# Kernel tuning notes

Measured on AMD Instinct MI355X. Metric: run time of the kernel, lower is better.

The kernel has to match this reference:

```python
import jax, jax.numpy as jnp
import numpy as np
import math

NUM_LEVEL = 16
LEVEL_DIM = 2
BASE_RES = 16
LOG2_T = 19
LEVEL_SCALE = 1.38191288
N_POINTS = 262144

_PRIMES = np.array([1, 2654435761, 805459861], dtype=np.uint32)  # tiny-cuda-nn hash primes
_CORNERS = np.array([[(c >> d) & 1 for d in range(3)] for c in range(8)], dtype=np.uint32)  # [8,3]


def _grid_meta():
    # mirrors GridEncoder.get_grid_info: per-level table offsets (aligned to 8)
    max_len = 2 ** LOG2_T
    offs = []
    off = 0
    for i in range(NUM_LEVEL):
        res = int(np.ceil(BASE_RES * LEVEL_SCALE ** i))
        p = min(max_len, res ** 3)
        p = int(np.ceil(p / 8) * 8)
        offs.append(off)
        off += p
    offs.append(off)
    return offs


def setup_inputs() -> dict:
    key = jax.random.key(0)
    k1, k2 = jax.random.split(key)
    offs = _grid_meta()
    # raw coords in [-1, 1); forward maps (x+1)/2 -> [0, 1)
    input_means = jax.random.uniform(k1, (N_POINTS, 3), dtype=jnp.float32) * 2.0 - 1.0
    # embeddings.data.uniform_(-0.01, 0.01)
    embeddings = jax.random.uniform(k2, (offs[-1], LEVEL_DIM), dtype=jnp.float32) * 0.02 - 0.01
    return {"input_means": input_means, "embeddings": embeddings}


def _encode(input_means, embeddings):
    x = (input_means + 1.0) / 2.0  # [N,3] in [0,1]
    offs = _grid_meta()
    lg_scale = math.log2(LEVEL_SCALE)
    corners = jnp.asarray(_CORNERS)  # [8,3]
    primes = jnp.asarray(_PRIMES)    # [3]
    outs = []
    for l in range(NUM_LEVEL):
        hsize = offs[l + 1] - offs[l]                    # table rows this level
        scale = 2.0 ** (l * lg_scale) * BASE_RES - 1.0   # align_corners=True
        res = int(math.ceil(scale)) + 1                  # grid resolution
        table = embeddings[offs[l]:offs[l + 1]]          # [hsize, C]
        pos = x * scale                                  # align_corners -> no +0.5
        pg = jnp.floor(pos)
        frac = pos - pg                                  # [N,3]
        pgu = pg.astype(jnp.uint32)
        cpos = pgu[:, None, :] + corners[None]           # [N,8,3] corner coords
        if res ** 3 > hsize:
            # hashed level: xor of coord*prime (uint32 wraparound)
            h = cpos * primes
            idx = h[..., 0] ^ h[..., 1] ^ h[..., 2]
        else:
            # dense (tiled) level
            r = jnp.uint32(res)
            idx = cpos[..., 0] + cpos[..., 1] * r + cpos[..., 2] * r * r
        idx = (idx % jnp.uint32(hsize)).astype(jnp.int32)
        feats = table[idx]                               # [N,8,C] gather
        w = jnp.where(corners[None] == 1, frac[:, None, :], 1.0 - frac[:, None, :]).prod(-1)  # [N,8]
        outs.append(jnp.einsum('nk,nkc->nc', w, feats))  # trilinear interp
    # matches ot_encod.permute(1,0,2).reshape(N, L*C): level-major feature concat
    return jnp.concatenate(outs, axis=-1)                # [N, L*C]


def reference(input_means, embeddings):
    return _encode(input_means, embeddings)
```

## Files before the change

kernel.cpp:

```cpp
#include <hip/hip_runtime.h>
#include <cmath>

#define NPTS 262144
#define NLVL 16
#define NDENSE 5
#define NHASH 11
#define HASH_MASK 0x7FFFFu

struct MetaD {
    float scale[NDENSE];
    unsigned off[NDENSE];
    unsigned res[NDENSE];
};
struct MetaH {
    float scale[NHASH];
    unsigned off[NHASH];
};

__global__ __launch_bounds__(256) void enc_dense(
    const float* __restrict__ means, const float* __restrict__ emb,
    float* __restrict__ out, MetaD meta)
{
    const int p = blockIdx.x * 256 + threadIdx.x;
    const int l = blockIdx.y;

    const float x = (means[3 * p + 0] + 1.0f) * 0.5f;
    const float y = (means[3 * p + 1] + 1.0f) * 0.5f;
    const float z = (means[3 * p + 2] + 1.0f) * 0.5f;

    const float s   = meta.scale[l];
    const unsigned off = meta.off[l];
    const unsigned r   = meta.res[l];

    const float px = x * s, py = y * s, pz = z * s;
    const float gx = floorf(px), gy = floorf(py), gz = floorf(pz);
    const float fx = px - gx, fy = py - gy, fz = pz - gz;
    const unsigned ix = (unsigned)gx, iy = (unsigned)gy, iz = (unsigned)gz;

    const unsigned base = ix + iy * r + iz * r * r + off;
    const unsigned dy = r, dz = r * r;

    const float2* __restrict__ emb2 = (const float2*)emb;
    float2 f[8];
    f[0] = emb2[base];
    f[1] = emb2[base + 1];
    f[2] = emb2[base + dy];
    f[3] = emb2[base + dy + 1];
    f[4] = emb2[base + dz];
    f[5] = emb2[base + dz + 1];
    f[6] = emb2[base + dz + dy];
    f[7] = emb2[base + dz + dy + 1];

    const float wx0 = 1.0f - fx, wy0 = 1.0f - fy, wz0 = 1.0f - fz;
    float a0 = 0.0f, a1 = 0.0f;
    {
        const float w00 = wz0 * wy0, w01 = wz0 * fy, w10 = fz * wy0, w11 = fz * fy;
        a0 = w00 * (wx0 * f[0].x + fx * f[1].x) + w01 * (wx0 * f[2].x + fx * f[3].x)
           + w10 * (wx0 * f[4].x + fx * f[5].x) + w11 * (wx0 * f[6].x + fx * f[7].x);
        a1 = w00 * (wx0 * f[0].y + fx * f[1].y) + w01 * (wx0 * f[2].y + fx * f[3].y)
           + w10 * (wx0 * f[4].y + fx * f[5].y) + w11 * (wx0 * f[6].y + fx * f[7].y);
    }

    float2* out2 = (float2*)out;
    out2[(size_t)p * NLVL + l] = make_float2(a0, a1);
}

__global__ __launch_bounds__(256) void enc_hash(
    const float* __restrict__ means, const float* __restrict__ emb,
    float* __restrict__ out, MetaH meta)
{
    const int p = blockIdx.x * 256 + threadIdx.x;
    const int l = blockIdx.y;

    const float x = (means[3 * p + 0] + 1.0f) * 0.5f;
    const float y = (means[3 * p + 1] + 1.0f) * 0.5f;
    const float z = (means[3 * p + 2] + 1.0f) * 0.5f;

    const float s    = meta.scale[l];
    const unsigned off = meta.off[l];

    const float px = x * s, py = y * s, pz = z * s;
    const float gx = floorf(px), gy = floorf(py), gz = floorf(pz);
    const float fx = px - gx, fy = py - gy, fz = pz - gz;
    const unsigned ix = (unsigned)gx, iy = (unsigned)gy, iz = (unsigned)gz;

    const unsigned hy0 = iy * 2654435761u;
    const unsigned hy1 = hy0 + 2654435761u;
    const unsigned hz0 = iz * 805459861u;
    const unsigned hz1 = hz0 + 805459861u;

    const float2* __restrict__ emb2 = (const float2*)emb;
    float2 f[8];
    f[0] = emb2[off + ((ix       ^ hy0 ^ hz0) & HASH_MASK)];
    f[1] = emb2[off + (((ix + 1) ^ hy0 ^ hz0) & HASH_MASK)];
    f[2] = emb2[off + ((ix       ^ hy1 ^ hz0) & HASH_MASK)];
    f[3] = emb2[off + (((ix + 1) ^ hy1 ^ hz0) & HASH_MASK)];
    f[4] = emb2[off + ((ix       ^ hy0 ^ hz1) & HASH_MASK)];
    f[5] = emb2[off + (((ix + 1) ^ hy0 ^ hz1) & HASH_MASK)];
    f[6] = emb2[off + ((ix       ^ hy1 ^ hz1) & HASH_MASK)];
    f[7] = emb2[off + (((ix + 1) ^ hy1 ^ hz1) & HASH_MASK)];

    const float wx0 = 1.0f - fx, wy0 = 1.0f - fy, wz0 = 1.0f - fz;
    float a0, a1;
    {
        const float w00 = wz0 * wy0, w01 = wz0 * fy, w10 = fz * wy0, w11 = fz * fy;
        a0 = w00 * (wx0 * f[0].x + fx * f[1].x) + w01 * (wx0 * f[2].x + fx * f[3].x)
           + w10 * (wx0 * f[4].x + fx * f[5].x) + w11 * (wx0 * f[6].x + fx * f[7].x);
        a1 = w00 * (wx0 * f[0].y + fx * f[1].y) + w01 * (wx0 * f[2].y + fx * f[3].y)
           + w10 * (wx0 * f[4].y + fx * f[5].y) + w11 * (wx0 * f[6].y + fx * f[7].y);
    }

    float2* out2 = (float2*)out;
    out2[(size_t)p * NLVL + (l + NDENSE)] = make_float2(a0, a1);
}

extern "C" void kernel_launch(void* const* d_in, const int* in_sizes, int n_in,
                              void* d_out, int out_size, void* d_ws, size_t ws_size,
                              hipStream_t stream)
{
    const float* means = (const float*)d_in[0];
    const float* emb   = (const float*)d_in[1];
    float* out         = (float*)d_out;

    MetaD md;
    MetaH mh;
    const double lg = log2(1.38191288);
    unsigned off = 0;
    for (int l = 0; l < NLVL; ++l) {
        const double scale_d = pow(2.0, (double)l * lg) * 16.0 - 1.0;
        const unsigned res_enc = (unsigned)ceil(scale_d) + 1u;

        const double gres_d = ceil(16.0 * pow(1.38191288, (double)l));
        unsigned long long r3 = (unsigned long long)gres_d;
        r3 = r3 * r3 * r3;
        unsigned long long pl = r3 < (1ull << 19) ? r3 : (1ull << 19);
        pl = (pl + 7ull) / 8ull * 8ull;

        if (l < NDENSE) {
            md.scale[l] = (float)scale_d;
            md.off[l]   = off;
            md.res[l]   = res_enc;
        } else {
            mh.scale[l - NDENSE] = (float)scale_d;
            mh.off[l - NDENSE]   = off;
        }
        off += (unsigned)pl;
    }

    dim3 blk(256, 1, 1);
    enc_dense<<<dim3(NPTS / 256, NDENSE, 1), blk, 0, stream>>>(means, emb, out, md);
    enc_hash <<<dim3(NPTS / 256, NHASH, 1), blk, 0, stream>>>(means, emb, out, mh);
}
```

Before: 247.6 us.

## Pin hash levels to XCDs, pair-load x-corners, stage level-major output

Hash-level blocks are remapped so each level's table is served by a fixed XCD (blockIdx & 7), which keeps each level's 4MB table resident in that XCD's L2. Levels 8-10 share pairs of XCDs. Each thread handles two points. When ix is even, the x-pair corners come from one float4 load, since XOR with an even hash keeps them adjacent. Output goes to a level-major workspace so stores are coalesced, then a transpose kernel writes the point-major result. This adds an extra kernel and extra global traffic for the transpose, and relies on the hardware dispatching blocks round-robin across XCDs.

```diff
diff --git a/kernel.cpp b/kernel.cpp
--- a/kernel.cpp
+++ b/kernel.cpp
@@ -7,19 +7,12 @@
 #define NHASH 11
 #define HASH_MASK 0x7FFFFu
 
-struct MetaD {
-    float scale[NDENSE];
-    unsigned off[NDENSE];
-    unsigned res[NDENSE];
-};
-struct MetaH {
-    float scale[NHASH];
-    unsigned off[NHASH];
-};
+struct MetaD { float scale[NDENSE]; unsigned off[NDENSE]; unsigned res[NDENSE]; };
+struct MetaH { float scale[NHASH]; unsigned off[NHASH]; };
 
 __global__ __launch_bounds__(256) void enc_dense(
     const float* __restrict__ means, const float* __restrict__ emb,
-    float* __restrict__ out, MetaD meta)
+    float2* __restrict__ dst, int lvl_major, MetaD meta)
 {
     const int p = blockIdx.x * 256 + threadIdx.x;
     const int l = blockIdx.y;
@@ -28,7 +21,7 @@
     const float y = (means[3 * p + 1] + 1.0f) * 0.5f;
     const float z = (means[3 * p + 2] + 1.0f) * 0.5f;
 
-    const float s   = meta.scale[l];
+    const float s      = meta.scale[l];
     const unsigned off = meta.off[l];
     const unsigned r   = meta.res[l];
 
@@ -42,76 +35,112 @@
 
     const float2* __restrict__ emb2 = (const float2*)emb;
     float2 f[8];
-    f[0] = emb2[base];
-    f[1] = emb2[base + 1];
-    f[2] = emb2[base + dy];
-    f[3] = emb2[base + dy + 1];
-    f[4] = emb2[base + dz];
-    f[5] = emb2[base + dz + 1];
-    f[6] = emb2[base + dz + dy];
-    f[7] = emb2[base + dz + dy + 1];
+    f[0] = emb2[base];           f[1] = emb2[base + 1];
+    f[2] = emb2[base + dy];      f[3] = emb2[base + dy + 1];
+    f[4] = emb2[base + dz];      f[5] = emb2[base + dz + 1];
+    f[6] = emb2[base + dz + dy]; f[7] = emb2[base + dz + dy + 1];
 
     const float wx0 = 1.0f - fx, wy0 = 1.0f - fy, wz0 = 1.0f - fz;
-    float a0 = 0.0f, a1 = 0.0f;
-    {
-        const float w00 = wz0 * wy0, w01 = wz0 * fy, w10 = fz * wy0, w11 = fz * fy;
-        a0 = w00 * (wx0 * f[0].x + fx * f[1].x) + w01 * (wx0 * f[2].x + fx * f[3].x)
-           + w10 * (wx0 * f[4].x + fx * f[5].x) + w11 * (wx0 * f[6].x + fx * f[7].x);
-        a1 = w00 * (wx0 * f[0].y + fx * f[1].y) + w01 * (wx0 * f[2].y + fx * f[3].y)
-           + w10 * (wx0 * f[4].y + fx * f[5].y) + w11 * (wx0 * f[6].y + fx * f[7].y);
-    }
+    const float w00 = wz0 * wy0, w01 = wz0 * fy, w10 = fz * wy0, w11 = fz * fy;
+    const float a0 = w00 * (wx0 * f[0].x + fx * f[1].x) + w01 * (wx0 * f[2].x + fx * f[3].x)
+                   + w10 * (wx0 * f[4].x + fx * f[5].x) + w11 * (wx0 * f[6].x + fx * f[7].x);
+    const float a1 = w00 * (wx0 * f[0].y + fx * f[1].y) + w01 * (wx0 * f[2].y + fx * f[3].y)
+                   + w10 * (wx0 * f[4].y + fx * f[5].y) + w11 * (wx0 * f[6].y + fx * f[7].y);
 
-    float2* out2 = (float2*)out;
-    out2[(size_t)p * NLVL + l] = make_float2(a0, a1);
+    const size_t di = lvl_major ? ((size_t)l * NPTS + p) : ((size_t)p * NLVL + l);
+    dst[di] = make_float2(a0, a1);
 }
 
-__global__ __launch_bounds__(256) void enc_hash(
-    const float* __restrict__ means, const float* __restrict__ emb,
-    float* __restrict__ out, MetaH meta)
+__device__ __forceinline__ float2 hash_level(
+    const float* __restrict__ emb, unsigned off, float s,
+    float x, float y, float z)
 {
-    const int p = blockIdx.x * 256 + threadIdx.x;
-    const int l = blockIdx.y;
-
-    const float x = (means[3 * p + 0] + 1.0f) * 0.5f;
-    const float y = (means[3 * p + 1] + 1.0f) * 0.5f;
-    const float z = (means[3 * p + 2] + 1.0f) * 0.5f;
-
-    const float s    = meta.scale[l];
-    const unsigned off = meta.off[l];
-
     const float px = x * s, py = y * s, pz = z * s;
     const float gx = floorf(px), gy = floorf(py), gz = floorf(pz);
     const float fx = px - gx, fy = py - gy, fz = pz - gz;
     const unsigned ix = (unsigned)gx, iy = (unsigned)gy, iz = (unsigned)gz;
 
-    const unsigned hy0 = iy * 2654435761u;
-    const unsigned hy1 = hy0 + 2654435761u;
-    const unsigned hz0 = iz * 805459861u;
-    const unsigned hz1 = hz0 + 805459861u;
+    const unsigned hy0 = iy * 2654435761u, hy1 = hy0 + 2654435761u;
+    const unsigned hz0 = iz * 805459861u,  hz1 = hz0 + 805459861u;
+    const unsigned hyz[4] = {hy0 ^ hz0, hy1 ^ hz0, hy0 ^ hz1, hy1 ^ hz1};
+
+    const float wy0 = 1.0f - fy, wz0 = 1.0f - fz;
+    const float wc[4] = {wy0 * wz0, fy * wz0, wy0 * fz, fy * fz};
+    const float wx0 = 1.0f - fx;
 
     const float2* __restrict__ emb2 = (const float2*)emb;
-    float2 f[8];
-    f[0] = emb2[off + ((ix       ^ hy0 ^ hz0) & HASH_MASK)];
-    f[1] = emb2[off + (((ix + 1) ^ hy0 ^ hz0) & HASH_MASK)];
-    f[2] = emb2[off + ((ix       ^ hy1 ^ hz0) & HASH_MASK)];
-    f[3] = emb2[off + (((ix + 1) ^ hy1 ^ hz0) & HASH_MASK)];
-    f[4] = emb2[off + ((ix       ^ hy0 ^ hz1) & HASH_MASK)];
-    f[5] = emb2[off + (((ix + 1) ^ hy0 ^ hz1) & HASH_MASK)];
-    f[6] = emb2[off + ((ix       ^ hy1 ^ hz1) & HASH_MASK)];
-    f[7] = emb2[off + (((ix + 1) ^ hy1 ^ hz1) & HASH_MASK)];
+    const float4* __restrict__ emb4 = (const float4*)emb;
 
-    const float wx0 = 1.0f - fx, wy0 = 1.0f - fy, wz0 = 1.0f - fz;
-    float a0, a1;
-    {
-        const float w00 = wz0 * wy0, w01 = wz0 * fy, w10 = fz * wy0, w11 = fz * fy;
-        a0 = w00 * (wx0 * f[0].x + fx * f[1].x) + w01 * (wx0 * f[2].x + fx * f[3].x)
-           + w10 * (wx0 * f[4].x + fx * f[5].x) + w11 * (wx0 * f[6].x + fx * f[7].x);
-        a1 = w00 * (wx0 * f[0].y + fx * f[1].y) + w01 * (wx0 * f[2].y + fx * f[3].y)
-           + w10 * (wx0 * f[4].y + fx * f[5].y) + w11 * (wx0 * f[6].y + fx * f[7].y);
+    float a0 = 0.0f, a1 = 0.0f;
+    if ((ix & 1u) == 0u) {
+#pragma unroll
+        for (int c = 0; c < 4; ++c) {
+            const unsigned i0 = (ix ^ hyz[c]) & HASH_MASK;
+            const float4 f = emb4[(off + (i0 & ~1u)) >> 1];
+            const bool sw = (i0 & 1u);
+            const float c0x = sw ? f.z : f.x, c0y = sw ? f.w : f.y;
+            const float c1x = sw ? f.x : f.z, c1y = sw ? f.y : f.w;
+            a0 += wc[c] * (wx0 * c0x + fx * c1x);
+            a1 += wc[c] * (wx0 * c0y + fx * c1y);
+        }
+    } else {
+#pragma unroll
+        for (int c = 0; c < 4; ++c) {
+            const unsigned i0 = (ix        ^ hyz[c]) & HASH_MASK;
+            const unsigned i1 = ((ix + 1u) ^ hyz[c]) & HASH_MASK;
+            const float2 f0 = emb2[off + i0];
+            const float2 f1 = emb2[off + i1];
+            a0 += wc[c] * (wx0 * f0.x + fx * f1.x);
+            a1 += wc[c] * (wx0 * f0.y + fx * f1.y);
+        }
     }
+    return make_float2(a0, a1);
+}
 
-    float2* out2 = (float2*)out;
-    out2[(size_t)p * NLVL + (l + NDENSE)] = make_float2(a0, a1);
+__global__ __launch_bounds__(256) void enc_hash(
+    const float* __restrict__ means, const float* __restrict__ emb,
+    float2* __restrict__ dst, int lvl_major, MetaH meta)
+{
+    const unsigned b = blockIdx.x;
+    const unsigned xcd = b & 7u, slot = b >> 3;
+    unsigned il, chunk;
+    if (slot < 512u) { il = xcd; chunk = slot; }
+    else {
+        if (xcd >= 6u) return;
+        il = 8u + (xcd >> 1);
+        chunk = ((slot - 512u) << 1) | (xcd & 1u);
+    }
+    const float s      = meta.scale[il];
+    const unsigned off = meta.off[il];
+    const unsigned lvl = il + NDENSE;
+
+    const unsigned p0 = chunk * 512u + threadIdx.x;
+
+#pragma unroll
+    for (int pp = 0; pp < 2; ++pp) {
+        const unsigned p = p0 + pp * 256u;
+        const float x = (means[3 * p + 0] + 1.0f) * 0.5f;
+        const float y = (means[3 * p + 1] + 1.0f) * 0.5f;
+        const float z = (means[3 * p + 2] + 1.0f) * 0.5f;
+        const float2 a = hash_level(emb, off, s, x, y, z);
+        const size_t di = lvl_major ? ((size_t)lvl * NPTS + p) : ((size_t)p * NLVL + lvl);
+        dst[di] = a;
+    }
+}
+
+__global__ __launch_bounds__(256) void transpose_out(
+    const float2* __restrict__ ws, float* __restrict__ out)
+{
+    const int p = blockIdx.x * 256 + threadIdx.x;
+    float4 o[8];
+    float2* o2 = (float2*)o;
+#pragma unroll
+    for (int l = 0; l < NLVL; ++l)
+        o2[l] = ws[(size_t)l * NPTS + p];
+    float4* out4 = (float4*)(out + (size_t)p * (2 * NLVL));
+#pragma unroll
+    for (int k = 0; k < 8; ++k)
+        out4[k] = o[k];
 }
 
 extern "C" void kernel_launch(void* const* d_in, const int* in_sizes, int n_in,
@@ -147,7 +176,13 @@
         off += (unsigned)pl;
     }
 
-    dim3 blk(256, 1, 1);
-    enc_dense<<<dim3(NPTS / 256, NDENSE, 1), blk, 0, stream>>>(means, emb, out, md);
-    enc_hash <<<dim3(NPTS / 256, NHASH, 1), blk, 0, stream>>>(means, emb, out, mh);
+    const size_t ws_needed = (size_t)NLVL * NPTS * sizeof(float2);
+    const bool use_ws = ws_size >= ws_needed;
+    float2* dst = use_ws ? (float2*)d_ws : (float2*)out;
+    const int lvl_major = use_ws ? 1 : 0;
+
+    enc_dense<<<dim3(NPTS / 256, NDENSE, 1), 256, 0, stream>>>(means, emb, dst, lvl_major, md);
+    enc_hash <<<dim3(8 * 768, 1, 1),          256, 0, stream>>>(means, emb, dst, lvl_major, mh);
+    if (use_ws)
+        transpose_out<<<NPTS / 256, 256, 0, stream>>>((const float2*)d_ws, out);
 }
```

New measurement: 204.0 us. 17.6% less time.
